# Kernel optimization log

Measured on AMD Instinct MI355X. Metric: run time of the kernel, lower is better.

Reference implementation:

```python
import jax, jax.numpy as jnp
import numpy as np

HIDDEN = 2048
N_EXPERTS = 8
TOP_K = 2
MOE_INTER = 1408
NORM_TOPK = False  # config.norm_topk_prob


def setup_inputs() -> dict:
    key = jax.random.key(0)
    k0, k1, k2, k3, k4 = jax.random.split(key, 5)
    hidden_states = jax.random.normal(k0, (2, 2048, HIDDEN), dtype=jnp.float32)
    # router gate: nn.Linear(hidden, num_experts, bias=False) -> store as [H, E]
    gate_w = jax.random.normal(k1, (HIDDEN, N_EXPERTS), dtype=jnp.float32) * 0.02
    # per-expert MLP weights, stacked over experts (Linear is x @ W.T, stored pre-transposed)
    w_gate = jax.random.normal(k2, (N_EXPERTS, HIDDEN, MOE_INTER), dtype=jnp.float32) * 0.02
    w_up = jax.random.normal(k3, (N_EXPERTS, HIDDEN, MOE_INTER), dtype=jnp.float32) * 0.02
    w_down = jax.random.normal(k4, (N_EXPERTS, MOE_INTER, HIDDEN), dtype=jnp.float32) * 0.02
    return {"hidden_states": hidden_states, "gate_w": gate_w,
            "w_gate": w_gate, "w_up": w_up, "w_down": w_down}


def reference(hidden_states, gate_w, w_gate, w_up, w_down):
    B, S, H = hidden_states.shape
    x = hidden_states.reshape(-1, H)                      # [T, H]
    T = x.shape[0]
    router_logits = x @ gate_w                            # [T, E]
    probs = jax.nn.softmax(router_logits.astype(jnp.float32), axis=-1)
    routing_weights, selected = jax.lax.top_k(probs, TOP_K)  # [T, K], [T, K]
    if NORM_TOPK:
        routing_weights = routing_weights / routing_weights.sum(-1, keepdims=True)
    routing_weights = routing_weights.astype(x.dtype)
    # dense combine weights [T, E]: scatter top-k weights to expert slots
    combine = jnp.zeros((T, N_EXPERTS), dtype=x.dtype)
    combine = combine.at[jnp.arange(T)[:, None], selected].add(routing_weights)
    # run all experts densely (reference form of gather-MLP-scatter)
    g = jnp.einsum('th,ehf->tef', x, w_gate)              # [T, E, F]
    u = jnp.einsum('th,ehf->tef', x, w_up)
    h = jax.nn.silu(g) * u
    y = jnp.einsum('tef,efh->teh', h, w_down)             # [T, E, H]
    out = jnp.einsum('te,teh->th', combine, y)            # [T, H]
    return out
```

## Files before the change

### kernel.cpp

```cpp
#include <hip/hip_runtime.h>
#include <hip/hip_bf16.h>

#define HID  2048
#define NEXP 8
#define FINT 1408
#define TM   128
#define BK   32
#define GU_NPAN 88
#define DN_NPAN 64

typedef __bf16 bf16_t;
typedef __bf16 bf16x8 __attribute__((ext_vector_type(8)));
typedef float  f32x4  __attribute__((ext_vector_type(4)));

#define AS1 __attribute__((address_space(1)))
#define AS3 __attribute__((address_space(3)))

__device__ __forceinline__ void gll16(const void* g, void* l) {
    __builtin_amdgcn_global_load_lds((const AS1 void*)g, (AS3 void*)l, 16, 0, 0);
}

#define VMCNT6() asm volatile("s_waitcnt vmcnt(6)" ::: "memory")
#define VMCNT0() asm volatile("s_waitcnt vmcnt(0)" ::: "memory")
#define SB0() __builtin_amdgcn_sched_barrier(0)

__global__ __launch_bounds__(64) void router_kernel(
    const float* __restrict__ x, const float* __restrict__ gw,
    int* __restrict__ cnt, int* __restrict__ topk_id, float* __restrict__ topk_w,
    bf16_t* __restrict__ xb, int T)
{
    int t = blockIdx.x;
    if (t >= T) return;
    int lane = threadIdx.x;
    float acc[NEXP];
#pragma unroll
    for (int e = 0; e < NEXP; ++e) acc[e] = 0.f;
    const float* xr = x + (size_t)t * HID;
    bf16_t* xo = xb + (size_t)t * HID;
    for (int i0 = lane * 4; i0 < HID; i0 += 256) {
        float4 xv = *(const float4*)(xr + i0);
        bf16_t b4[4] = {(bf16_t)xv.x, (bf16_t)xv.y, (bf16_t)xv.z, (bf16_t)xv.w};
        *(uint2*)(xo + i0) = *(uint2*)b4;
        float xs[4] = {xv.x, xv.y, xv.z, xv.w};
#pragma unroll
        for (int u = 0; u < 4; ++u) {
            const float4* g4 = (const float4*)(gw + (size_t)(i0 + u) * NEXP);
            float4 a = g4[0], b = g4[1];
            acc[0] += xs[u] * a.x; acc[1] += xs[u] * a.y; acc[2] += xs[u] * a.z; acc[3] += xs[u] * a.w;
            acc[4] += xs[u] * b.x; acc[5] += xs[u] * b.y; acc[6] += xs[u] * b.z; acc[7] += xs[u] * b.w;
        }
    }
#pragma unroll
    for (int d = 1; d < 64; d <<= 1) {
#pragma unroll
        for (int e = 0; e < NEXP; ++e) acc[e] += __shfl_xor(acc[e], d, 64);
    }
    float mx = acc[0];
#pragma unroll
    for (int e = 1; e < NEXP; ++e) mx = fmaxf(mx, acc[e]);
    float p[NEXP]; float s = 0.f;
#pragma unroll
    for (int e = 0; e < NEXP; ++e) { p[e] = expf(acc[e] - mx); s += p[e]; }
    float inv = 1.f / s;
    int i1 = 0;
#pragma unroll
    for (int e = 1; e < NEXP; ++e) if (acc[e] > acc[i1]) i1 = e;
    int i2 = (i1 == 0) ? 1 : 0;
#pragma unroll
    for (int e = 0; e < NEXP; ++e) if (e != i1 && acc[e] > acc[i2]) i2 = e;
    if (lane == 0) {
        topk_id[t * 2 + 0] = i1; topk_id[t * 2 + 1] = i2;
        topk_w[t * 2 + 0] = p[i1] * inv; topk_w[t * 2 + 1] = p[i2] * inv;
        atomicAdd(&cnt[i1], 1); atomicAdd(&cnt[i2], 1);
    }
}

__global__ void offsets_kernel(const int* __restrict__ cnt, int* __restrict__ offs,
                               int* __restrict__ gbase, int* __restrict__ gcount,
                               int* __restrict__ dbase, int* __restrict__ dcount,
                               int* __restrict__ gu, int* __restrict__ dn)
{
    __shared__ int gc[8], dc[8];
    int tid = threadIdx.x;
    if (tid == 0) {
        int s = 0;
        for (int e = 0; e < NEXP; ++e) { offs[e] = s; s += cnt[e]; }
        offs[NEXP] = s;
    }
    if (tid < 8) {
        int c = 0;
        for (int p = tid; p < GU_NPAN; p += 8) { int e = p / 11; c += (cnt[e] + TM - 1) / TM; }
        gc[tid] = c;
    } else if (tid < 16) {
        int x = tid - 8, c = 0;
        for (int p = x; p < DN_NPAN; p += 8) { int e = p >> 3; c += (cnt[e] + TM - 1) / TM; }
        dc[x] = c;
    }
    __syncthreads();
    if (tid < 8) {
        int base = 0;
        for (int i = 0; i < tid; ++i) base += gc[i];
        gbase[tid] = base; gcount[tid] = gc[tid];
        int k = base;
        for (int p = tid; p < GU_NPAN; p += 8) {
            int e = p / 11, fp = p - e * 11;
            int nt = (cnt[e] + TM - 1) / TM;
            for (int t = 0; t < nt; ++t) gu[k++] = (e << 10) | (fp << 6) | t;
        }
    } else if (tid < 16) {
        int x = tid - 8;
        int base = 0;
        for (int i = 0; i < x; ++i) base += dc[i];
        dbase[x] = base; dcount[x] = dc[x];
        int k = base;
        for (int p = x; p < DN_NPAN; p += 8) {
            int e = p >> 3, hp = p & 7;
            int nt = (cnt[e] + TM - 1) / TM;
            for (int t = 0; t < nt; ++t) dn[k++] = (e << 10) | (hp << 6) | t;
        }
    }
}

__global__ void scatter_kernel(
    const int* __restrict__ topk_id, const int* __restrict__ offs, int* __restrict__ fill,
    int* __restrict__ tok, int* __restrict__ slot_of, int T)
{
    int t = blockIdx.x * blockDim.x + threadIdx.x;
    if (t >= T) return;
#pragma unroll
    for (int k = 0; k < 2; ++k) {
        int e = topk_id[t * 2 + k];
        int pos = atomicAdd(&fill[e], 1);
        int slot = offs[e] + pos;
        tok[slot] = t;
        slot_of[t * 2 + k] = slot;
    }
}

__global__ __launch_bounds__(256) void cvt3_kernel(
    const float* __restrict__ wg, const float* __restrict__ wu, const float* __restrict__ wd,
    bf16_t* __restrict__ wgb, bf16_t* __restrict__ wub, bf16_t* __restrict__ wdb)
{
    const int per = NEXP * (HID / 64) * (FINT / 64);
    int b = blockIdx.x;
    const float* in; bf16_t* outb; int R, C;
    if (b < per)            { in = wg; outb = wgb; R = HID;  C = FINT; }
    else if (b < 2 * per)   { b -= per; in = wu; outb = wub; R = HID;  C = FINT; }
    else                    { b -= 2 * per; in = wd; outb = wdb; R = FINT; C = HID; }

    int tilesC = C >> 6;
    int perE = (R >> 6) * tilesC;
    int e = b / perE;
    int rem = b - e * perE;
    int tr = rem / tilesC, tc = rem - tr * tilesC;
    const float* src = in + (size_t)e * R * C + (size_t)(tr * 64) * C + tc * 64;
    bf16_t* dst = outb + (size_t)e * R * C + (size_t)(tc * 64) * R + tr * 64;

    __shared__ float tile[64][65];
    int tid = threadIdx.x;
    int rr = tid >> 4;
    int cc = (tid & 15) * 4;
#pragma unroll
    for (int i = 0; i < 4; ++i) {
        float4 v = *(const float4*)(src + (size_t)(rr + i * 16) * C + cc);
        tile[rr + i * 16][cc + 0] = v.x; tile[rr + i * 16][cc + 1] = v.y;
        tile[rr + i * 16][cc + 2] = v.z; tile[rr + i * 16][cc + 3] = v.w;
    }
    __syncthreads();
    int oc = tid >> 2;
    int og = (tid & 3) * 16;
    bf16_t* dp = dst + (size_t)oc * R + og;
    bf16x8 o0, o1;
#pragma unroll
    for (int j = 0; j < 8; ++j) { o0[j] = (bf16_t)tile[og + j][oc]; o1[j] = (bf16_t)tile[og + 8 + j][oc]; }
    *(bf16x8*)dp = o0;
    *(bf16x8*)(dp + 8) = o1;
}

__global__ __launch_bounds__(256, 2) void gateup3_kernel(
    const bf16_t* __restrict__ xb, const bf16_t* __restrict__ wgb, const bf16_t* __restrict__ wub,
    const int* __restrict__ offs, const int* __restrict__ tok,
    const int* __restrict__ gbase, const int* __restrict__ gcount, const int* __restrict__ gu,
    bf16_t* __restrict__ h_buf)
{
    __shared__ bf16_t smem[36864];
    const int tid = threadIdx.x;
    const int lane = tid & 63, w = tid >> 6;
    const int lr = lane & 15, lg = lane >> 4;
    const int rl = lane >> 2;
    const int sw8 = ((lane & 3) ^ ((lane >> 3) & 3)) * 8;
    const int ksw = (lg ^ ((lr >> 1) & 3)) * 8;

    const int xcd = blockIdx.x & 7, slot = blockIdx.x >> 3;
    const int icnt = gcount[xcd], ib = gbase[xcd];

    for (int ii = slot; ii < icnt; ii += 96) {
        const int it = gu[ib + ii];
        const int e = it >> 10, fp = (it >> 6) & 15, tr = it & 63;
        const int seg0 = offs[e];
        const int rbase = tr * TM;
        const int nvalid = min(offs[e + 1] - seg0 - rbase, TM);
        const int row0 = seg0 + rbase;
        const int f0 = fp * 128;

        const bf16_t* aP[2];
#pragma unroll
        for (int i = 0; i < 2; ++i) {
            int r = w * 32 + i * 16 + rl;
            int tk = tok[row0 + min(r, nvalid - 1)];
            aP[i] = xb + (size_t)tk * HID + sw8;
        }
        const bf16_t* bP[4];
#pragma unroll
        for (int j = 0; j < 4; ++j) {
            int br = w * 64 + j * 16 + rl;
            const bf16_t* W = (br < 128) ? wgb : wub;
            bP[j] = W + ((size_t)e * FINT + f0 + (br & 127)) * HID + sw8;
        }

        f32x4 acc[8][4];
#pragma unroll
        for (int mi = 0; mi < 8; ++mi)
#pragma unroll
            for (int ni = 0; ni < 4; ++ni) acc[mi][ni] = (f32x4){0.f, 0.f, 0.f, 0.f};

        auto STAGE = [&](int b, int kt) {
            int k0 = kt * BK;
            bf16_t* A = smem + b * 4096;
            bf16_t* B = smem + 12288 + b * 8192;
            gll16(aP[0] + k0, A + (w * 2 + 0) * 512);
            gll16(aP[1] + k0, A + (w * 2 + 1) * 512);
            gll16(bP[0] + k0, B + (w * 4 + 0) * 512);
            gll16(bP[1] + k0, B + (w * 4 + 1) * 512);
            gll16(bP[2] + k0, B + (w * 4 + 2) * 512);
            gll16(bP[3] + k0, B + (w * 4 + 3) * 512);
        };
        auto COMPUTE = [&](int b) {
            const bf16_t* A = smem + b * 4096;
            const bf16_t* B = smem + 12288 + b * 8192;
            bf16x8 bfr[4];
#pragma unroll
            for (int ni = 0; ni < 4; ++ni)
                bfr[ni] = *(const bf16x8*)&B[(w * 64 + ni * 16 + lr) * BK + ksw];
#pragma unroll
            for (int mi = 0; mi < 8; ++mi) {
                bf16x8 a = *(const bf16x8*)&A[(mi * 16 + lr) * BK + ksw];
#pragma unroll
                for (int ni = 0; ni < 4; ++ni)
                    acc[mi][ni] = __builtin_amdgcn_mfma_f32_16x16x32_bf16(a, bfr[ni], acc[mi][ni], 0, 0, 0);
            }
        };

        const int NK = HID / BK;
        STAGE(0, 0); STAGE(1, 1);
        int c0 = 0, c1 = 1, c2 = 2;
        for (int kt = 0; kt < NK - 1; ++kt) {
            SB0(); VMCNT6(); __builtin_amdgcn_s_barrier(); SB0();
            if (kt + 2 < NK) STAGE(c2, kt + 2);
            SB0();
            COMPUTE(c0);
            int t = c0; c0 = c1; c1 = c2; c2 = t;
        }
        SB0(); VMCNT0(); __builtin_amdgcn_s_barrier(); SB0();
        COMPUTE(c0);
        __syncthreads();

        if (w >= 2) {
#pragma unroll
            for (int mi = 0; mi < 8; ++mi)
#pragma unroll
                for (int ni = 0; ni < 4; ++ni)
#pragma unroll
                    for (int rr = 0; rr < 4; ++rr) {
                        int row = mi * 16 + lg * 4 + rr;
                        int col = (w - 2) * 64 + ni * 16 + lr;
                        smem[row * 128 + col] = (bf16_t)acc[mi][ni][rr];
                    }
        }
        __syncthreads();
        if (w < 2) {
#pragma unroll
            for (int mi = 0; mi < 8; ++mi)
#pragma unroll
                for (int ni = 0; ni < 4; ++ni)
#pragma unroll
                    for (int rr = 0; rr < 4; ++rr) {
                        int row = mi * 16 + lg * 4 + rr;
                        int col = w * 64 + ni * 16 + lr;
                        float g = acc[mi][ni][rr];
                        float u = (float)smem[row * 128 + col];
                        float h = (g / (1.f + __expf(-g))) * u;
                        if (row < nvalid)
                            h_buf[(size_t)(row0 + row) * FINT + f0 + col] = (bf16_t)h;
                    }
        }
        __syncthreads();
    }
}

__global__ __launch_bounds__(256, 2) void down3_kernel(
    const bf16_t* __restrict__ h_buf, const bf16_t* __restrict__ wdb,
    const int* __restrict__ offs,
    const int* __restrict__ dbase, const int* __restrict__ dcount, const int* __restrict__ dn,
    bf16_t* __restrict__ y_buf)
{
    __shared__ bf16_t smem[36864];
    const int tid = threadIdx.x;
    const int lane = tid & 63, w = tid >> 6;
    const int lr = lane & 15, lg = lane >> 4;
    const int rl = lane >> 2;
    const int sw8 = ((lane & 3) ^ ((lane >> 3) & 3)) * 8;
    const int ksw = (lg ^ ((lr >> 1) & 3)) * 8;

    const int xcd = blockIdx.x & 7, slot = blockIdx.x >> 3;
    const int icnt = dcount[xcd], ib = dbase[xcd];

    for (int ii = slot; ii < icnt; ii += 96) {
        const int it = dn[ib + ii];
        const int e = it >> 10, hp = (it >> 6) & 15, tr = it & 63;
        const int seg0 = offs[e];
        const int rbase = tr * TM;
        const int nvalid = min(offs[e + 1] - seg0 - rbase, TM);
        const int row0 = seg0 + rbase;
        const int h0 = hp * 256;

        const bf16_t* aP[2];
#pragma unroll
        for (int i = 0; i < 2; ++i) {
            int r = w * 32 + i * 16 + rl;
            aP[i] = h_buf + (size_t)(row0 + min(r, nvalid - 1)) * FINT + sw8;
        }
        const bf16_t* bP[4];
#pragma unroll
        for (int j = 0; j < 4; ++j) {
            int br = w * 64 + j * 16 + rl;
            bP[j] = wdb + ((size_t)e * HID + h0 + br) * FINT + sw8;
        }

        f32x4 acc[8][4];
#pragma unroll
        for (int mi = 0; mi < 8; ++mi)
#pragma unroll
            for (int ni = 0; ni < 4; ++ni) acc[mi][ni] = (f32x4){0.f, 0.f, 0.f, 0.f};

        auto STAGE = [&](int b, int kt) {
            int k0 = kt * BK;
            bf16_t* A = smem + b * 4096;
            bf16_t* B = smem + 12288 + b * 8192;
            gll16(aP[0] + k0, A + (w * 2 + 0) * 512);
            gll16(aP[1] + k0, A + (w * 2 + 1) * 512);
            gll16(bP[0] + k0, B + (w * 4 + 0) * 512);
            gll16(bP[1] + k0, B + (w * 4 + 1) * 512);
            gll16(bP[2] + k0, B + (w * 4 + 2) * 512);
            gll16(bP[3] + k0, B + (w * 4 + 3) * 512);
        };
        auto COMPUTE = [&](int b) {
            const bf16_t* A = smem + b * 4096;
            const bf16_t* B = smem + 12288 + b * 8192;
            bf16x8 bfr[4];
#pragma unroll
            for (int ni = 0; ni < 4; ++ni)
                bfr[ni] = *(const bf16x8*)&B[(w * 64 + ni * 16 + lr) * BK + ksw];
#pragma unroll
            for (int mi = 0; mi < 8; ++mi) {
                bf16x8 a = *(const bf16x8*)&A[(mi * 16 + lr) * BK + ksw];
#pragma unroll
                for (int ni = 0; ni < 4; ++ni)
                    acc[mi][ni] = __builtin_amdgcn_mfma_f32_16x16x32_bf16(a, bfr[ni], acc[mi][ni], 0, 0, 0);
            }
        };

        const int NK = FINT / BK;
        STAGE(0, 0); STAGE(1, 1);
        int c0 = 0, c1 = 1, c2 = 2;
        for (int kt = 0; kt < NK - 1; ++kt) {
            SB0(); VMCNT6(); __builtin_amdgcn_s_barrier(); SB0();
            if (kt + 2 < NK) STAGE(c2, kt + 2);
            SB0();
            COMPUTE(c0);
            int t = c0; c0 = c1; c1 = c2; c2 = t;
        }
        SB0(); VMCNT0(); __builtin_amdgcn_s_barrier(); SB0();
        COMPUTE(c0);

#pragma unroll
        for (int mi = 0; mi < 8; ++mi)
#pragma unroll
            for (int ni = 0; ni < 4; ++ni)
#pragma unroll
                for (int rr = 0; rr < 4; ++rr) {
                    int row = mi * 16 + lg * 4 + rr;
                    int col = w * 64 + ni * 16 + lr;
                    if (row < nvalid)
                        y_buf[(size_t)(row0 + row) * HID + h0 + col] = (bf16_t)acc[mi][ni][rr];
                }
        __syncthreads();
    }
}

__global__ __launch_bounds__(256) void combine_kernel(
    const bf16_t* __restrict__ y, const int* __restrict__ slot_of,
    const float* __restrict__ topk_w, float* __restrict__ out, int T)
{
    int t = blockIdx.x;
    int tid = threadIdx.x;
    int s0 = slot_of[t * 2], s1 = slot_of[t * 2 + 1];
    float w0 = topk_w[t * 2], w1 = topk_w[t * 2 + 1];
    const bf16x8* y0 = (const bf16x8*)(y + (size_t)s0 * HID);
    const bf16x8* y1 = (const bf16x8*)(y + (size_t)s1 * HID);
    bf16x8 v0 = y0[tid], v1 = y1[tid];
    float* op = out + (size_t)t * HID + tid * 8;
#pragma unroll
    for (int j = 0; j < 8; ++j)
        op[j] = w0 * (float)v0[j] + w1 * (float)v1[j];
}

extern "C" void kernel_launch(void* const* d_in, const int* in_sizes, int n_in,
                              void* d_out, int out_size, void* d_ws, size_t ws_size,
                              hipStream_t stream)
{
    const float* x  = (const float*)d_in[0];
    const float* gw = (const float*)d_in[1];
    const float* wg = (const float*)d_in[2];
    const float* wu = (const float*)d_in[3];
    const float* wd = (const float*)d_in[4];
    float* out = (float*)d_out;
    int T = in_sizes[0] / HID;
    int S2 = 2 * T;

    char* base = (char*)d_ws;
    int* cnt     = (int*)base;
    int* fill    = cnt + 8;
    int* offs    = cnt + 16;
    int* gbase   = cnt + 32;
    int* gcount  = cnt + 40;
    int* dbase   = cnt + 48;
    int* dcount  = cnt + 56;
    int* gu      = cnt + 64;
    int* dnl     = cnt + 1088;
    int* topk_id = cnt + 1856;
    float* topk_w = (float*)(topk_id + S2);
    int* tok     = (int*)(topk_w + S2);
    int* slot_of = tok + S2 + 256;
    size_t small_end = (size_t)((char*)(slot_of + S2) - base);
    size_t cur = (small_end + 255) & ~(size_t)255;
    auto take = [&](size_t bytes) -> size_t {
        size_t o = cur; cur += bytes; cur = (cur + 255) & ~(size_t)255; return o;
    };
    size_t wbytes = (size_t)NEXP * HID * FINT * 2;
    size_t o_xb  = take((size_t)T * HID * 2);
    size_t o_wgb = take(wbytes);
    size_t o_wub = take(wbytes);
    size_t o_wdb = take(wbytes);
    size_t o_h   = take((size_t)(S2 + 256) * FINT * 2);
    size_t o_y   = take((size_t)(S2 + 256) * HID * 2);
    (void)ws_size;

    bf16_t* xb    = (bf16_t*)(base + o_xb);
    bf16_t* wgb   = (bf16_t*)(base + o_wgb);
    bf16_t* wub   = (bf16_t*)(base + o_wub);
    bf16_t* wdb   = (bf16_t*)(base + o_wdb);
    bf16_t* h_buf = (bf16_t*)(base + o_h);
    bf16_t* y_buf = (bf16_t*)(base + o_y);

    hipMemsetAsync(base, 0, 64, stream);

    router_kernel<<<T, 64, 0, stream>>>(x, gw, cnt, topk_id, topk_w, xb, T);
    offsets_kernel<<<1, 64, 0, stream>>>(cnt, offs, gbase, gcount, dbase, dcount, gu, dnl);
    scatter_kernel<<<(T + 255) / 256, 256, 0, stream>>>(topk_id, offs, fill, tok, slot_of, T);

    int gridW = 3 * NEXP * (HID / 64) * (FINT / 64);
    cvt3_kernel<<<gridW, 256, 0, stream>>>(wg, wu, wd, wgb, wub, wdb);

    gateup3_kernel<<<768, 256, 0, stream>>>(xb, wgb, wub, offs, tok, gbase, gcount, gu, h_buf);
    down3_kernel<<<768, 256, 0, stream>>>(h_buf, wdb, offs, dbase, dcount, dnl, y_buf);
    combine_kernel<<<T, 256, 0, stream>>>(y_buf, slot_of, topk_w, out, T);
}
```

Baseline: 462.8 us.

## Pre-tile weights into LDS-ready swizzled blocks and resize GEMM grids

The weight conversion kernel now writes gate/up and down weights in a pre-tiled, pre-swizzled layout. Each 32-wide k-slice for a 128-column gate+up panel, or a 256-column down panel, becomes one contiguous 16KB block. The GEMM kernels then stage B tiles with fully contiguous per-lane loads instead of strided row gathers. Grid sizes and the per-XCD loop stride change from 768/96 to 704/88 and 512/64 so each block handles one work item per pass. Conversion still runs every call, and the new transpose adds LDS reads that may hit bank conflicts.

```diff
diff --git a/kernel.cpp b/kernel.cpp
--- a/kernel.cpp
+++ b/kernel.cpp
@@ -8,6 +8,8 @@
 #define BK   32
 #define GU_NPAN 88
 #define DN_NPAN 64
+#define NG_GU (NEXP * 11 * 64)
+#define NG_DN (NEXP * 8 * 44)
 
 typedef __bf16 bf16_t;
 typedef __bf16 bf16x8 __attribute__((ext_vector_type(8)));
@@ -137,48 +139,80 @@
     }
 }
 
-__global__ __launch_bounds__(256) void cvt3_kernel(
+__global__ __launch_bounds__(256) void cvtW_kernel(
     const float* __restrict__ wg, const float* __restrict__ wu, const float* __restrict__ wd,
-    bf16_t* __restrict__ wgb, bf16_t* __restrict__ wub, bf16_t* __restrict__ wdb)
-{
-    const int per = NEXP * (HID / 64) * (FINT / 64);
+    bf16_t* __restrict__ wB, bf16_t* __restrict__ wD)
+{
     int b = blockIdx.x;
-    const float* in; bf16_t* outb; int R, C;
-    if (b < per)            { in = wg; outb = wgb; R = HID;  C = FINT; }
-    else if (b < 2 * per)   { b -= per; in = wu; outb = wub; R = HID;  C = FINT; }
-    else                    { b -= 2 * per; in = wd; outb = wdb; R = FINT; C = HID; }
-
-    int tilesC = C >> 6;
-    int perE = (R >> 6) * tilesC;
-    int e = b / perE;
-    int rem = b - e * perE;
-    int tr = rem / tilesC, tc = rem - tr * tilesC;
-    const float* src = in + (size_t)e * R * C + (size_t)(tr * 64) * C + tc * 64;
-    bf16_t* dst = outb + (size_t)e * R * C + (size_t)(tc * 64) * R + tr * 64;
-
-    __shared__ float tile[64][65];
-    int tid = threadIdx.x;
-    int rr = tid >> 4;
-    int cc = (tid & 15) * 4;
-#pragma unroll
-    for (int i = 0; i < 4; ++i) {
-        float4 v = *(const float4*)(src + (size_t)(rr + i * 16) * C + cc);
-        tile[rr + i * 16][cc + 0] = v.x; tile[rr + i * 16][cc + 1] = v.y;
-        tile[rr + i * 16][cc + 2] = v.z; tile[rr + i * 16][cc + 3] = v.w;
-    }
-    __syncthreads();
-    int oc = tid >> 2;
-    int og = (tid & 3) * 16;
-    bf16_t* dp = dst + (size_t)oc * R + og;
-    bf16x8 o0, o1;
-#pragma unroll
-    for (int j = 0; j < 8; ++j) { o0[j] = (bf16_t)tile[og + j][oc]; o1[j] = (bf16_t)tile[og + 8 + j][oc]; }
-    *(bf16x8*)dp = o0;
-    *(bf16x8*)(dp + 8) = o1;
+    int t = threadIdx.x;
+    if (b < NG_GU) {
+        __shared__ bf16_t lg[32][136], lu[32][136];
+        int e = b / 704, rem = b - e * 704;
+        int fp = rem / 64, kt = rem - fp * 64;
+        int hh = t >> 3, cf = (t & 7) * 16;
+        const float* gsrc = wg + ((size_t)e * HID + kt * 32 + hh) * FINT + fp * 128 + cf;
+        const float* usrc = wu + ((size_t)e * HID + kt * 32 + hh) * FINT + fp * 128 + cf;
+#pragma unroll
+        for (int i = 0; i < 4; ++i) {
+            float4 v = *(const float4*)(gsrc + i * 4);
+            lg[hh][cf + i * 4 + 0] = (bf16_t)v.x; lg[hh][cf + i * 4 + 1] = (bf16_t)v.y;
+            lg[hh][cf + i * 4 + 2] = (bf16_t)v.z; lg[hh][cf + i * 4 + 3] = (bf16_t)v.w;
+        }
+#pragma unroll
+        for (int i = 0; i < 4; ++i) {
+            float4 v = *(const float4*)(usrc + i * 4);
+            lu[hh][cf + i * 4 + 0] = (bf16_t)v.x; lu[hh][cf + i * 4 + 1] = (bf16_t)v.y;
+            lu[hh][cf + i * 4 + 2] = (bf16_t)v.z; lu[hh][cf + i * 4 + 3] = (bf16_t)v.w;
+        }
+        __syncthreads();
+        int g = t >> 4, rl = t & 15;
+        int fcol = (g * 16 + rl) & 127;
+        int swz = (rl >> 1) & 3;
+        bf16_t o[32];
+        if (g < 8) {
+#pragma unroll
+            for (int c = 0; c < 4; ++c)
+#pragma unroll
+                for (int q = 0; q < 8; ++q) o[c * 8 + q] = lg[(c ^ swz) * 8 + q][fcol];
+        } else {
+#pragma unroll
+            for (int c = 0; c < 4; ++c)
+#pragma unroll
+                for (int q = 0; q < 8; ++q) o[c * 8 + q] = lu[(c ^ swz) * 8 + q][fcol];
+        }
+        bf16_t* dst = wB + (size_t)b * 8192 + t * 32;
+#pragma unroll
+        for (int i = 0; i < 4; ++i) *(bf16x8*)(dst + i * 8) = *(bf16x8*)(o + i * 8);
+    } else {
+        __shared__ bf16_t ld[32][264];
+        int b2 = b - NG_GU;
+        int e = b2 / 352, rem = b2 - e * 352;
+        int hp = rem / 44, kt = rem - hp * 44;
+        int ff = t >> 3, ch = (t & 7) * 32;
+        const float* dsrc = wd + ((size_t)e * FINT + kt * 32 + ff) * HID + hp * 256 + ch;
+#pragma unroll
+        for (int i = 0; i < 8; ++i) {
+            float4 v = *(const float4*)(dsrc + i * 4);
+            ld[ff][ch + i * 4 + 0] = (bf16_t)v.x; ld[ff][ch + i * 4 + 1] = (bf16_t)v.y;
+            ld[ff][ch + i * 4 + 2] = (bf16_t)v.z; ld[ff][ch + i * 4 + 3] = (bf16_t)v.w;
+        }
+        __syncthreads();
+        int g = t >> 4, rl = t & 15;
+        int hcol = g * 16 + rl;
+        int swz = (rl >> 1) & 3;
+        bf16_t o[32];
+#pragma unroll
+        for (int c = 0; c < 4; ++c)
+#pragma unroll
+            for (int q = 0; q < 8; ++q) o[c * 8 + q] = ld[(c ^ swz) * 8 + q][hcol];
+        bf16_t* dst = wD + (size_t)b2 * 8192 + t * 32;
+#pragma unroll
+        for (int i = 0; i < 4; ++i) *(bf16x8*)(dst + i * 8) = *(bf16x8*)(o + i * 8);
+    }
 }
 
 __global__ __launch_bounds__(256, 2) void gateup3_kernel(
-    const bf16_t* __restrict__ xb, const bf16_t* __restrict__ wgb, const bf16_t* __restrict__ wub,
+    const bf16_t* __restrict__ xb, const bf16_t* __restrict__ wB,
     const int* __restrict__ offs, const int* __restrict__ tok,
     const int* __restrict__ gbase, const int* __restrict__ gcount, const int* __restrict__ gu,
     bf16_t* __restrict__ h_buf)
@@ -194,7 +228,7 @@
     const int xcd = blockIdx.x & 7, slot = blockIdx.x >> 3;
     const int icnt = gcount[xcd], ib = gbase[xcd];
 
-    for (int ii = slot; ii < icnt; ii += 96) {
+    for (int ii = slot; ii < icnt; ii += 88) {
         const int it = gu[ib + ii];
         const int e = it >> 10, fp = (it >> 6) & 15, tr = it & 63;
         const int seg0 = offs[e];
@@ -210,13 +244,7 @@
             int tk = tok[row0 + min(r, nvalid - 1)];
             aP[i] = xb + (size_t)tk * HID + sw8;
         }
-        const bf16_t* bP[4];
-#pragma unroll
-        for (int j = 0; j < 4; ++j) {
-            int br = w * 64 + j * 16 + rl;
-            const bf16_t* W = (br < 128) ? wgb : wub;
-            bP[j] = W + ((size_t)e * FINT + f0 + (br & 127)) * HID + sw8;
-        }
+        const bf16_t* bT = wB + (size_t)(e * 11 + fp) * 64 * 8192 + lane * 8;
 
         f32x4 acc[8][4];
 #pragma unroll
@@ -230,10 +258,11 @@
             bf16_t* B = smem + 12288 + b * 8192;
             gll16(aP[0] + k0, A + (w * 2 + 0) * 512);
             gll16(aP[1] + k0, A + (w * 2 + 1) * 512);
-            gll16(bP[0] + k0, B + (w * 4 + 0) * 512);
-            gll16(bP[1] + k0, B + (w * 4 + 1) * 512);
-            gll16(bP[2] + k0, B + (w * 4 + 2) * 512);
-            gll16(bP[3] + k0, B + (w * 4 + 3) * 512);
+            const bf16_t* bk = bT + (size_t)kt * 8192;
+            gll16(bk + (w * 4 + 0) * 512, B + (w * 4 + 0) * 512);
+            gll16(bk + (w * 4 + 1) * 512, B + (w * 4 + 1) * 512);
+            gll16(bk + (w * 4 + 2) * 512, B + (w * 4 + 2) * 512);
+            gll16(bk + (w * 4 + 3) * 512, B + (w * 4 + 3) * 512);
         };
         auto COMPUTE = [&](int b) {
             const bf16_t* A = smem + b * 4096;
@@ -299,7 +328,7 @@
 }
 
 __global__ __launch_bounds__(256, 2) void down3_kernel(
-    const bf16_t* __restrict__ h_buf, const bf16_t* __restrict__ wdb,
+    const bf16_t* __restrict__ h_buf, const bf16_t* __restrict__ wD,
     const int* __restrict__ offs,
     const int* __restrict__ dbase, const int* __restrict__ dcount, const int* __restrict__ dn,
     bf16_t* __restrict__ y_buf)
@@ -315,7 +344,7 @@
     const int xcd = blockIdx.x & 7, slot = blockIdx.x >> 3;
     const int icnt = dcount[xcd], ib = dbase[xcd];
 
-    for (int ii = slot; ii < icnt; ii += 96) {
+    for (int ii = slot; ii < icnt; ii += 64) {
         const int it = dn[ib + ii];
         const int e = it >> 10, hp = (it >> 6) & 15, tr = it & 63;
         const int seg0 = offs[e];
@@ -330,12 +359,7 @@
             int r = w * 32 + i * 16 + rl;
             aP[i] = h_buf + (size_t)(row0 + min(r, nvalid - 1)) * FINT + sw8;
         }
-        const bf16_t* bP[4];
-#pragma unroll
-        for (int j = 0; j < 4; ++j) {
-            int br = w * 64 + j * 16 + rl;
-            bP[j] = wdb + ((size_t)e * HID + h0 + br) * FINT + sw8;
-        }
+        const bf16_t* bT = wD + (size_t)(e * 8 + hp) * 44 * 8192 + lane * 8;
 
         f32x4 acc[8][4];
 #pragma unroll
@@ -349,10 +373,11 @@
             bf16_t* B = smem + 12288 + b * 8192;
             gll16(aP[0] + k0, A + (w * 2 + 0) * 512);
             gll16(aP[1] + k0, A + (w * 2 + 1) * 512);
-            gll16(bP[0] + k0, B + (w * 4 + 0) * 512);
-            gll16(bP[1] + k0, B + (w * 4 + 1) * 512);
-            gll16(bP[2] + k0, B + (w * 4 + 2) * 512);
-            gll16(bP[3] + k0, B + (w * 4 + 3) * 512);
+            const bf16_t* bk = bT + (size_t)kt * 8192;
+            gll16(bk + (w * 4 + 0) * 512, B + (w * 4 + 0) * 512);
+            gll16(bk + (w * 4 + 1) * 512, B + (w * 4 + 1) * 512);
+            gll16(bk + (w * 4 + 2) * 512, B + (w * 4 + 2) * 512);
+            gll16(bk + (w * 4 + 3) * 512, B + (w * 4 + 3) * 512);
         };
         auto COMPUTE = [&](int b) {
             const bf16_t* A = smem + b * 4096;
@@ -447,19 +472,16 @@
     auto take = [&](size_t bytes) -> size_t {
         size_t o = cur; cur += bytes; cur = (cur + 255) & ~(size_t)255; return o;
     };
-    size_t wbytes = (size_t)NEXP * HID * FINT * 2;
-    size_t o_xb  = take((size_t)T * HID * 2);
-    size_t o_wgb = take(wbytes);
-    size_t o_wub = take(wbytes);
-    size_t o_wdb = take(wbytes);
-    size_t o_h   = take((size_t)(S2 + 256) * FINT * 2);
-    size_t o_y   = take((size_t)(S2 + 256) * HID * 2);
+    size_t o_xb = take((size_t)T * HID * 2);
+    size_t o_wB = take((size_t)NG_GU * 8192 * 2);
+    size_t o_wD = take((size_t)NG_DN * 8192 * 2);
+    size_t o_h  = take((size_t)(S2 + 256) * FINT * 2);
+    size_t o_y  = take((size_t)(S2 + 256) * HID * 2);
     (void)ws_size;
 
     bf16_t* xb    = (bf16_t*)(base + o_xb);
-    bf16_t* wgb   = (bf16_t*)(base + o_wgb);
-    bf16_t* wub   = (bf16_t*)(base + o_wub);
-    bf16_t* wdb   = (bf16_t*)(base + o_wdb);
+    bf16_t* wB    = (bf16_t*)(base + o_wB);
+    bf16_t* wD    = (bf16_t*)(base + o_wD);
     bf16_t* h_buf = (bf16_t*)(base + o_h);
     bf16_t* y_buf = (bf16_t*)(base + o_y);
 
@@ -469,10 +491,9 @@
     offsets_kernel<<<1, 64, 0, stream>>>(cnt, offs, gbase, gcount, dbase, dcount, gu, dnl);
     scatter_kernel<<<(T + 255) / 256, 256, 0, stream>>>(topk_id, offs, fill, tok, slot_of, T);
 
-    int gridW = 3 * NEXP * (HID / 64) * (FINT / 64);
-    cvt3_kernel<<<gridW, 256, 0, stream>>>(wg, wu, wd, wgb, wub, wdb);
-
-    gateup3_kernel<<<768, 256, 0, stream>>>(xb, wgb, wub, offs, tok, gbase, gcount, gu, h_buf);
-    down3_kernel<<<768, 256, 0, stream>>>(h_buf, wdb, offs, dbase, dcount, dnl, y_buf);
+    cvtW_kernel<<<NG_GU + NG_DN, 256, 0, stream>>>(wg, wu, wd, wB, wD);
+
+    gateup3_kernel<<<704, 256, 0, stream>>>(xb, wB, offs, tok, gbase, gcount, gu, h_buf);
+    down3_kernel<<<512, 256, 0, stream>>>(h_buf, wD, offs, dbase, dcount, dnl, y_buf);
     combine_kernel<<<T, 256, 0, stream>>>(y_buf, slot_of, topk_w, out, T);
 }
```

Result: no change. 459.2 us (-0.8%).
